# Kernel optimization log

Hardware: AMD Instinct MI355X
Metric: run time of the kernel (lower is better)

The kernel has to match this reference:

```python
import jax, jax.numpy as jnp
import numpy as np

B, S, V, D, F, NC = 256, 64, 100000, 64, 10, 10  # batch, seq, vocab, emb_dim, n_feats, n_clusters


def setup_inputs() -> dict:
    key = jax.random.key(0)
    ks = jax.random.split(key, 12)
    ids = jax.random.randint(ks[0], (B, S), 0, V)
    emb_table = jax.random.normal(ks[1], (V, D), dtype=jnp.float32) * 0.02
    comb_w1 = jax.random.normal(ks[2], (2 * D, D), dtype=jnp.float32) / np.sqrt(2 * D)
    comb_b1 = jnp.zeros((D,), jnp.float32)
    comb_w2 = jax.random.normal(ks[3], (D, F), dtype=jnp.float32) / np.sqrt(D)
    comb_b2 = jnp.zeros((F,), jnp.float32)
    freq_w1 = jax.random.normal(ks[4], (D + 1, D), dtype=jnp.float32) / np.sqrt(D + 1)
    freq_b1 = jnp.zeros((D,), jnp.float32)
    freq_w2 = jax.random.normal(ks[5], (D, F), dtype=jnp.float32) / np.sqrt(D)
    freq_b2 = jnp.zeros((F,), jnp.float32)
    cluster_centers = jax.random.normal(ks[6], (NC, D), dtype=jnp.float32)
    cat_freq = jnp.ones((V,), jnp.float32)          # category_frequencies buffer
    total_samples = jnp.array(1.0, jnp.float32)     # total_samples buffer
    return dict(category_ids=ids, emb_table=emb_table,
                comb_w1=comb_w1, comb_b1=comb_b1, comb_w2=comb_w2, comb_b2=comb_b2,
                freq_w1=freq_w1, freq_b1=freq_b1, freq_w2=freq_w2, freq_b2=freq_b2,
                cluster_centers=cluster_centers, cat_freq=cat_freq,
                total_samples=total_samples)


def reference(category_ids, emb_table, comb_w1, comb_b1, comb_w2, comb_b2,
              freq_w1, freq_b1, freq_w2, freq_b2, cluster_centers,
              cat_freq, total_samples):
    emb = emb_table[category_ids]                      # [B,S,D]
    # --- pairwise combination features (vectorized over all i<j pairs) ---
    iu, ju = np.triu_indices(S, 1)                     # P = S*(S-1)/2 pairs
    P = iu.shape[0]
    pairs = jnp.concatenate([emb[:, iu], emb[:, ju]], axis=-1)   # [B,P,2D]
    h = jax.nn.relu(jnp.einsum('bpe,ed->bpd', pairs, comb_w1) + comb_b1)
    combo = jnp.einsum('bpd,df->bpf', h, comb_w2) + comb_b2      # [B,P,F]
    combo_sum = combo.sum(axis=1)                      # [B,F]
    # --- frequency features ---
    freqs = cat_freq[category_ids] / total_samples     # [B,S]
    freq_in = jnp.concatenate([emb, freqs[..., None]], axis=-1)  # [B,S,D+1]
    fh = jax.nn.relu(jnp.einsum('bse,ed->bsd', freq_in, freq_w1) + freq_b1)
    freq_feat = jnp.einsum('bsd,df->bsf', fh, freq_w2) + freq_b2  # [B,S,F]
    # --- cluster assignment features (softmax over -euclidean distances) ---
    d2 = (jnp.sum(emb * emb, axis=-1, keepdims=True)
          + jnp.sum(cluster_centers * cluster_centers, axis=-1)
          - 2.0 * jnp.einsum('bsd,cd->bsc', emb, cluster_centers))
    dist = jnp.sqrt(jnp.maximum(d2, 0.0))              # [B,S,NC]
    cluster_feat = jax.nn.softmax(-dist, axis=-1)      # [B,S,F] (F==NC)
    # --- mean over stacked features: freq + P pair feats (broadcast over seq) + cluster ---
    out = (freq_feat + combo_sum[:, None, :] + cluster_feat) / (P + 2)
    return out
```

## Files before the change

kernel.cpp:

```cpp
#include <hip/hip_runtime.h>
#include <math.h>


typedef _Float16 h2 __attribute__((ext_vector_type(2)));
typedef _Float16 h4 __attribute__((ext_vector_type(4)));
typedef _Float16 h8 __attribute__((ext_vector_type(8)));
union H4u { h4 v; h2 h[2]; };
union H8u { h8 v; h2 h[4]; };

constexpr int BATCH = 256;
constexpr int S = 64, D = 64, F = 10;
constexpr int NPAIR = S * (S - 1) / 2;

constexpr int EMBS = 6144;
constexpr int U2B  = 8448;
constexpr int V2T  = 10496;
constexpr int FHT  = 12608;
constexpr int DI_F = 14784;
constexpr int W2P  = 15424;
constexpr int PART_F = 0;
constexpr int FF_F   = 2048;
constexpr int CS_F   = 2752;

__device__ __forceinline__ h2 pk2(float a, float b) {
#if __has_builtin(__builtin_amdgcn_cvt_pkrtz)
  auto t = __builtin_amdgcn_cvt_pkrtz(a, b);
  return __builtin_bit_cast(h2, t);
#else
  h2 r; r.x = (_Float16)a; r.y = (_Float16)b; return r;
#endif
}

__device__ __forceinline__ float fdot2f(h2 a, h2 b, float c) {
#if __has_builtin(__builtin_amdgcn_fdot2)
  typedef __fp16 q2 __attribute__((ext_vector_type(2)));
  return __builtin_amdgcn_fdot2(__builtin_bit_cast(q2, a),
                                __builtin_bit_cast(q2, b), c, false);
#else
  return c + (float)a.x * (float)b.x + (float)a.y * (float)b.y;
#endif
}

__device__ __forceinline__ h2 hmax2z(h2 a) {
#if __has_builtin(__builtin_elementwise_max)
  h2 z = {(_Float16)0, (_Float16)0};
  return __builtin_elementwise_max(a, z);
#else
  h2 r;
  r.x = a.x > (_Float16)0 ? a.x : (_Float16)0;
  r.y = a.y > (_Float16)0 ? a.y : (_Float16)0;
  return r;
#endif
}

__device__ __forceinline__ float lane_up1(float v) {
#if __has_builtin(__builtin_amdgcn_update_dpp)
  int r = __builtin_amdgcn_update_dpp(0, __float_as_int(v), 0xF5, 0xF, 0xF, false);
  return __int_as_float(r);
#else
  return __shfl_down(v, 1, 64);
#endif
}

__global__ __launch_bounds__(1024, 4)
void cat_enc_kernel(const int*   __restrict__ ids,
                    const float* __restrict__ emb_table,
                    const float* __restrict__ comb_w1,
                    const float* __restrict__ comb_b1,
                    const float* __restrict__ comb_w2,
                    const float* __restrict__ comb_b2,
                    const float* __restrict__ freq_w1,
                    const float* __restrict__ freq_b1,
                    const float* __restrict__ freq_w2,
                    const float* __restrict__ freq_b2,
                    const float* __restrict__ centers,
                    const float* __restrict__ cat_freq,
                    const float* __restrict__ total_samples,
                    float*       __restrict__ out)
{
  __shared__ __align__(16) unsigned int ldsu[15744];
  h2*    ldsH = (h2*)ldsu;
  float* ldsf = (float*)ldsu;
  const int tid = threadIdx.x;
  const int b = blockIdx.x, bBase = b * S;

  {
    int s = tid >> 4, q = tid & 15;
    int id = ids[bBase + s];
    float4 e4 = *(const float4*)(emb_table + (size_t)id * D + q * 4);
    H4u ep; ep.h[0] = pk2(e4.x, e4.y); ep.h[1] = pk2(e4.z, e4.w);
    *(h4*)&ldsH[EMBS + s * 36 + q * 2] = ep.v;

    {
      const int k4 = tid >> 6, dd = tid & 63;
      const float* s0p = comb_w1 + (k4 * 4) * D + dd;
      const float* s1p = s0p + D * D;
      const float* s2p = freq_w1 + (k4 * 4) * D + dd;
      h4* dst = (h4*)ldsu;
      H4u u0; u0.h[0] = pk2(s0p[0], s0p[D]); u0.h[1] = pk2(s0p[2 * D], s0p[3 * D]);
      H4u u1; u1.h[0] = pk2(s1p[0], s1p[D]); u1.h[1] = pk2(s1p[2 * D], s1p[3 * D]);
      H4u u2; u2.h[0] = pk2(s2p[0], s2p[D]); u2.h[1] = pk2(s2p[2 * D], s2p[3 * D]);
      dst[2 * tid]     = u0.v;
      dst[2 * tid + 1] = u1.v;
      dst[2048 + tid]  = u2.v;
    }
    if (tid < 320) {
      int f = tid >> 5, d2 = tid & 31;
      ldsH[W2P + tid] = pk2(freq_w2[(2 * d2) * F + f], freq_w2[(2 * d2 + 1) * F + f]);
    }
  }
  __syncthreads();

  {
    const int wv   = __builtin_amdgcn_readfirstlane((int)(tid >> 6));
    const int lane = tid & 63;
    if (wv < 8) {
      const int d  = lane;
      const int s0 = wv * 8;
      const float invT = 1.0f / total_samples[0];
      const float b1d = comb_b1[d], fb1d = freq_b1[d], fw1L = freq_w1[D * D + d];
      float aU[8], aV[8], aF[8];
#pragma unroll
      for (int si = 0; si < 8; ++si) {
        int idv = __builtin_amdgcn_readfirstlane(ids[bBase + s0 + si]);
        aU[si] = b1d; aV[si] = 0.f;
        aF[si] = fmaf(cat_freq[idv] * invT, fw1L, fb1d);
      }
      const h8* WUVp = (const h8*)ldsu;
      const h4* WFp  = (const h4*)(ldsu + 4096);
#pragma unroll 2
      for (int k8 = 0; k8 < 8; ++k8) {
        H8u wa; wa.v = WUVp[(2 * k8) * 64 + d];
        H8u wb; wb.v = WUVp[(2 * k8 + 1) * 64 + d];
        H4u fa; fa.v = WFp[(2 * k8) * 64 + d];
        H4u fb; fb.v = WFp[(2 * k8 + 1) * 64 + d];
#pragma unroll
        for (int si = 0; si < 8; ++si) {
          H8u e; e.v = *(const h8*)&ldsH[EMBS + (s0 + si) * 36 + k8 * 4];
          aU[si] = fdot2f(e.h[0], wa.h[0], aU[si]);
          aU[si] = fdot2f(e.h[1], wa.h[1], aU[si]);
          aV[si] = fdot2f(e.h[0], wa.h[2], aV[si]);
          aV[si] = fdot2f(e.h[1], wa.h[3], aV[si]);
          aF[si] = fdot2f(e.h[0], fa.h[0], aF[si]);
          aF[si] = fdot2f(e.h[1], fa.h[1], aF[si]);
          aU[si] = fdot2f(e.h[2], wb.h[0], aU[si]);
          aU[si] = fdot2f(e.h[3], wb.h[1], aU[si]);
          aV[si] = fdot2f(e.h[2], wb.h[2], aV[si]);
          aV[si] = fdot2f(e.h[3], wb.h[3], aV[si]);
          aF[si] = fdot2f(e.h[2], fb.h[0], aF[si]);
          aF[si] = fdot2f(e.h[3], fb.h[1], aF[si]);
        }
      }
      const bool evenl = ((d & 1) == 0);
      const int d2 = d >> 1;
#pragma unroll
      for (int si = 0; si < 8; ++si) {
        float un = lane_up1(aU[si]);
        float vn = lane_up1(aV[si]);
        float fh = fmaxf(aF[si], 0.f);
        float fn = lane_up1(fh);
        if (evenl) {
          int srow = s0 + si;
          ldsH[U2B + srow * 32 + d2] = pk2(aU[si], un);
          ldsH[V2T + d2 * 66 + srow] = pk2(aV[si], vn);
          ldsH[FHT + srow * 34 + d2] = pk2(fh, fn);
        }
      }
    } else {
      const int s = lane;
      H8u er[8];
#pragma unroll
      for (int k8 = 0; k8 < 8; ++k8)
        er[k8].v = *(const h8*)&ldsH[EMBS + s * 36 + k8 * 4];
      for (int cc = wv - 8; cc < 10; cc += 8) {
        const float* crow = centers + cc * D;
        float acc = 0.f;
#pragma unroll
        for (int k8 = 0; k8 < 8; ++k8) {
#pragma unroll
          for (int t = 0; t < 4; ++t) {
            const int k2 = k8 * 4 + t;
            float t0 = (float)er[k8].h[t].x - crow[2 * k2];
            float t1 = (float)er[k8].h[t].y - crow[2 * k2 + 1];
            acc = fmaf(t0, t0, fmaf(t1, t1, acc));
          }
        }
        ldsf[DI_F + s * 10 + cc] = sqrtf(acc);
      }
    }
  }
  __syncthreads();

  {
    if (tid < 640) {
      int s = tid & 63;
      int f = __builtin_amdgcn_readfirstlane((int)(tid >> 6));
      float acc = freq_b2[f];
      const h8* wrow = (const h8*)&ldsH[W2P + f * 32];
#pragma unroll
      for (int d8 = 0; d8 < 4; ++d8) {
        H8u wf; wf.v = wrow[d8];
        H4u f0; f0.v = *(const h4*)&ldsH[FHT + s * 34 + d8 * 4];
        H4u f1; f1.v = *(const h4*)&ldsH[FHT + s * 34 + d8 * 4 + 2];
        acc = fdot2f(f0.h[0], wf.h[0], acc);
        acc = fdot2f(f0.h[1], wf.h[1], acc);
        acc = fdot2f(f1.h[0], wf.h[2], acc);
        acc = fdot2f(f1.h[1], wf.h[3], acc);
      }
      ldsf[FF_F + s * 10 + f] = acc;
    } else if (tid < 704) {
      int s = tid - 640;
      float dv[10], dmin = 1e30f;
#pragma unroll
      for (int c = 0; c < 10; ++c) { dv[c] = ldsf[DI_F + s * 10 + c]; dmin = fminf(dmin, dv[c]); }
      float p[10], sum = 0.f;
#pragma unroll
      for (int c = 0; c < 10; ++c) { p[c] = expf(dmin - dv[c]); sum += p[c]; }
      float rs = 1.0f / sum;
#pragma unroll
      for (int c = 0; c < 10; ++c) ldsf[DI_F + s * 10 + c] = p[c] * rs;
    }
  }

  {
    const int dg = tid & 31, g = tid >> 5;
    h2 u2a = ldsH[U2B + g * 32 + dg];
    h2 u2b = ldsH[U2B + (63 - g) * 32 + dg];
    h2 za = {(_Float16)0, (_Float16)0};
    h2 acA0 = za, acA1 = za, accb = za;
    const int jsplit = 64 - g;
    int j = g + 1;
    if (j & 1) {
      h2 v2 = ldsH[V2T + dg * 66 + j];
      acA0 = acA0 + hmax2z(u2a + v2);
      ++j;
    }
#pragma unroll 4
    for (; j < 64; j += 2) {
      H4u v; v.v = *(const h4*)&ldsH[V2T + dg * 66 + j];
      acA0 = acA0 + hmax2z(u2a + v.h[0]);
      acA1 = acA1 + hmax2z(u2a + v.h[1]);
      if (j + 1 >= jsplit) {
        if (j >= jsplit) accb = accb + hmax2z(u2b + v.h[0]);
        accb = accb + hmax2z(u2b + v.h[1]);
      }
    }
    h2 at = acA0 + acA1 + accb;
    ldsf[PART_F + g * 64 + 2 * dg]     = (float)at.x;
    ldsf[PART_F + g * 64 + 2 * dg + 1] = (float)at.y;
  }
  __syncthreads();

  if (tid < 64) {
    float h = 0.f;
#pragma unroll
    for (int g2 = 0; g2 < 32; ++g2) h += ldsf[PART_F + g2 * 64 + tid];
    float csv = 0.f;
#pragma unroll
    for (int f = 0; f < 10; ++f) {
      float p = h * comb_w2[tid * F + f];
#pragma unroll
      for (int off = 1; off < 64; off <<= 1) p += __shfl_xor(p, off, 64);
      if (tid == f) csv = p;
    }
    if (tid < 10) ldsf[CS_F + tid] = fmaf(comb_b2[tid], (float)NPAIR, csv);
  }
  __syncthreads();

  if (tid < 640) {
    int f = tid % 10;
    float val = (ldsf[FF_F + tid] + ldsf[CS_F + f] + ldsf[DI_F + tid])
              * (1.0f / (float)(NPAIR + 2));
    out[(size_t)b * 640 + tid] = val;
  }
}

extern "C" void kernel_launch(void* const* d_in, const int* in_sizes, int n_in,
                              void* d_out, int out_size, void* d_ws, size_t ws_size,
                              hipStream_t stream) {
  (void)in_sizes; (void)n_in; (void)d_ws; (void)ws_size; (void)out_size;
  const int*   ids        = (const int*)  d_in[0];
  const float* emb_table  = (const float*)d_in[1];
  const float* comb_w1    = (const float*)d_in[2];
  const float* comb_b1    = (const float*)d_in[3];
  const float* comb_w2    = (const float*)d_in[4];
  const float* comb_b2    = (const float*)d_in[5];
  const float* freq_w1    = (const float*)d_in[6];
  const float* freq_b1    = (const float*)d_in[7];
  const float* freq_w2    = (const float*)d_in[8];
  const float* freq_b2    = (const float*)d_in[9];
  const float* centers    = (const float*)d_in[10];
  const float* cat_freq   = (const float*)d_in[11];
  const float* total_samp = (const float*)d_in[12];
  float* out = (float*)d_out;

  hipLaunchKernelGGL(cat_enc_kernel, dim3(BATCH), dim3(1024), 0, stream,
                     ids, emb_table, comb_w1, comb_b1, comb_w2, comb_b2,
                     freq_w1, freq_b1, freq_w2, freq_b2, centers, cat_freq,
                     total_samp, out);
}
```

Before: 109.4 us.

## Fuse combo reduction, softmax and output into one parallel epilogue

Cuts one barrier by merging the combo-sum projection, the cluster softmax and the output write into a single 640-thread stage, where each wave handles one feature. The freq-MLP result now stays in a register instead of going through LDS. Category frequencies are staged in LDS during the embedding load, replacing scalar global loads. Each thread recomputes the 10-way softmax sum, which adds redundant expf work, the DI stride is padded to 11, and output stores are now strided rather than contiguous.

After: 107.7 us. No clear change (-1.6%).

```diff
diff --git a/kernel.cpp b/kernel.cpp
--- a/kernel.cpp
+++ b/kernel.cpp
@@ -17,10 +17,9 @@
 constexpr int V2T  = 10496;
 constexpr int FHT  = 12608;
 constexpr int DI_F = 14784;
-constexpr int W2P  = 15424;
+constexpr int W2P  = 15488;
+constexpr int FRQ  = 15808;
 constexpr int PART_F = 0;
-constexpr int FF_F   = 2048;
-constexpr int CS_F   = 2752;
 
 __device__ __forceinline__ h2 pk2(float a, float b) {
 #if __has_builtin(__builtin_amdgcn_cvt_pkrtz)
@@ -78,11 +77,12 @@
                     const float* __restrict__ total_samples,
                     float*       __restrict__ out)
 {
-  __shared__ __align__(16) unsigned int ldsu[15744];
+  __shared__ __align__(16) unsigned int ldsu[15872];
   h2*    ldsH = (h2*)ldsu;
   float* ldsf = (float*)ldsu;
   const int tid = threadIdx.x;
   const int b = blockIdx.x, bBase = b * S;
+  float ffreg = 0.f;
 
   {
     int s = tid >> 4, q = tid & 15;
@@ -90,6 +90,7 @@
     float4 e4 = *(const float4*)(emb_table + (size_t)id * D + q * 4);
     H4u ep; ep.h[0] = pk2(e4.x, e4.y); ep.h[1] = pk2(e4.z, e4.w);
     *(h4*)&ldsH[EMBS + s * 36 + q * 2] = ep.v;
+    if (q == 0) ldsf[FRQ + s] = cat_freq[id];
 
     {
       const int k4 = tid >> 6, dd = tid & 63;
@@ -122,9 +123,8 @@
       float aU[8], aV[8], aF[8];
 #pragma unroll
       for (int si = 0; si < 8; ++si) {
-        int idv = __builtin_amdgcn_readfirstlane(ids[bBase + s0 + si]);
         aU[si] = b1d; aV[si] = 0.f;
-        aF[si] = fmaf(cat_freq[idv] * invT, fw1L, fb1d);
+        aF[si] = fmaf(ldsf[FRQ + s0 + si] * invT, fw1L, fb1d);
       }
       const h8* WUVp = (const h8*)ldsu;
       const h4* WFp  = (const h4*)(ldsu + 4096);
@@ -185,7 +185,7 @@
             acc = fmaf(t0, t0, fmaf(t1, t1, acc));
           }
         }
-        ldsf[DI_F + s * 10 + cc] = sqrtf(acc);
+        ldsf[DI_F + s * 11 + cc] = sqrtf(acc);
       }
     }
   }
@@ -207,18 +207,7 @@
         acc = fdot2f(f1.h[0], wf.h[2], acc);
         acc = fdot2f(f1.h[1], wf.h[3], acc);
       }
-      ldsf[FF_F + s * 10 + f] = acc;
-    } else if (tid < 704) {
-      int s = tid - 640;
-      float dv[10], dmin = 1e30f;
-#pragma unroll
-      for (int c = 0; c < 10; ++c) { dv[c] = ldsf[DI_F + s * 10 + c]; dmin = fminf(dmin, dv[c]); }
-      float p[10], sum = 0.f;
-#pragma unroll
-      for (int c = 0; c < 10; ++c) { p[c] = expf(dmin - dv[c]); sum += p[c]; }
-      float rs = 1.0f / sum;
-#pragma unroll
-      for (int c = 0; c < 10; ++c) ldsf[DI_F + s * 10 + c] = p[c] * rs;
+      ffreg = acc;
     }
   }
 
@@ -251,27 +240,25 @@
   }
   __syncthreads();
 
-  if (tid < 64) {
+  if (tid < 640) {
+    const int f = __builtin_amdgcn_readfirstlane((int)(tid >> 6));
+    const int l = tid & 63;
     float h = 0.f;
 #pragma unroll
-    for (int g2 = 0; g2 < 32; ++g2) h += ldsf[PART_F + g2 * 64 + tid];
-    float csv = 0.f;
-#pragma unroll
-    for (int f = 0; f < 10; ++f) {
-      float p = h * comb_w2[tid * F + f];
-#pragma unroll
-      for (int off = 1; off < 64; off <<= 1) p += __shfl_xor(p, off, 64);
-      if (tid == f) csv = p;
-    }
-    if (tid < 10) ldsf[CS_F + tid] = fmaf(comb_b2[tid], (float)NPAIR, csv);
-  }
-  __syncthreads();
-
-  if (tid < 640) {
-    int f = tid % 10;
-    float val = (ldsf[FF_F + tid] + ldsf[CS_F + f] + ldsf[DI_F + tid])
-              * (1.0f / (float)(NPAIR + 2));
-    out[(size_t)b * 640 + tid] = val;
+    for (int g2 = 0; g2 < 32; ++g2) h += ldsf[PART_F + g2 * 64 + l];
+    float p = h * comb_w2[l * F + f];
+#pragma unroll
+    for (int off = 1; off < 64; off <<= 1) p += __shfl_xor(p, off, 64);
+    const float cs = fmaf(comb_b2[f], (float)NPAIR, p);
+    float dv[10], dmin = 1e30f;
+#pragma unroll
+    for (int c = 0; c < 10; ++c) { dv[c] = ldsf[DI_F + l * 11 + c]; dmin = fminf(dmin, dv[c]); }
+    float sum = 0.f;
+#pragma unroll
+    for (int c = 0; c < 10; ++c) sum += expf(dmin - dv[c]);
+    const float clu = expf(dmin - dv[f]) / sum;
+    const float val = (ffreg + cs + clu) * (1.0f / (float)(NPAIR + 2));
+    out[(size_t)b * 640 + l * 10 + f] = val;
   }
 }
 
```
